# Kernel optimization log

Measured on AMD Instinct MI355X. Metric: run time of the kernel, lower is better.

## Reference

```python
import jax, jax.numpy as jnp
import numpy as np

# Model hyperparameters (match init_kwargs)
NUM_HEADS = 12
KEY_SIZE = 64
VALUE_SIZE = 64
D_MODEL = 768
NUM_LAYERS = 4
FFW = 3072
B, T, L = 2, 32, 256
LN_EPS = 1e-5


def _layer_norm(x, scale, offset):
    m = jnp.mean(x, axis=-1, keepdims=True)
    v = jnp.mean(jnp.square(x - m), axis=-1, keepdims=True)
    return (x - m) * jax.lax.rsqrt(v + LN_EPS) * scale + offset


def _axial_attn(x, Wq, Wk, Wv, Wo, bo, mode):
    # x: [B, T, L, D]
    b, t, l, d = x.shape
    q = (x @ Wq).reshape(b, t, l, NUM_HEADS, KEY_SIZE)
    k = (x @ Wk).reshape(b, t, l, NUM_HEADS, KEY_SIZE)
    v = (x @ Wv).reshape(b, t, l, NUM_HEADS, VALUE_SIZE)
    inv_sqrt_d = KEY_SIZE ** (-0.5)
    if mode == 'time':
        logits = jnp.einsum('btlhd,bTlhd->blhtT', q, k) * inv_sqrt_d
        w = jax.nn.softmax(logits, axis=-1)
        a = jnp.einsum('blhtT,bTlhd->btlhd', w, v)
    else:  # space
        logits = jnp.einsum('btlhd,btLhd->bthlL', q, k) * inv_sqrt_d
        w = jax.nn.softmax(logits, axis=-1)
        a = jnp.einsum('bthlL,btLhd->btlhd', w, v)
    a = a.reshape(b, t, l, NUM_HEADS * VALUE_SIZE)
    return a @ Wo + bo


def _forward(input_embeddings, Wq_t, Wk_t, Wv_t, Wo_t, bo_t,
             Wq_s, Wk_s, Wv_s, Wo_s, bo_s,
             ln_t_scale, ln_t_bias, ln_s_scale, ln_s_bias,
             ln2_scale, ln2_bias, W1, b1, W2, b2):
    def block(h, p):
        (wq_t, wk_t, wv_t, wo_t, bot, wq_s, wk_s, wv_s, wo_s, bos,
         lts, ltb, lss, lsb, l2s, l2b, w1, bb1, w2, bb2) = p
        # time attention + residual
        x = _layer_norm(h, lts, ltb)
        h = h + _axial_attn(x, wq_t, wk_t, wv_t, wo_t, bot, 'time')
        # space attention + residual
        x = _layer_norm(h, lss, lsb)
        h = h + _axial_attn(x, wq_s, wk_s, wv_s, wo_s, bos, 'space')
        # FFN + residual
        x = _layer_norm(h, l2s, l2b)
        ff = jax.nn.gelu(x @ w1 + bb1) @ w2 + bb2
        return h + ff, None

    params = (Wq_t, Wk_t, Wv_t, Wo_t, bo_t, Wq_s, Wk_s, Wv_s, Wo_s, bo_s,
              ln_t_scale, ln_t_bias, ln_s_scale, ln_s_bias,
              ln2_scale, ln2_bias, W1, b1, W2, b2)
    h, _ = jax.lax.scan(block, input_embeddings, params)
    return h


def setup_inputs() -> dict:
    key = jax.random.key(0)
    ks = jax.random.split(key, 32)
    D, H, KD, VD, F, NL = D_MODEL, NUM_HEADS, KEY_SIZE, VALUE_SIZE, FFW, NUM_LAYERS
    init_scale = 2.0 / np.sqrt(NL)  # VarianceScaling scale used by the module
    s_in = np.sqrt(init_scale / D).astype(np.float32)   # fan_in = D
    s_out = np.sqrt(init_scale / (H * VD)).astype(np.float32)
    s_ffw2 = np.sqrt(init_scale / F).astype(np.float32)
    x = jax.random.normal(ks[0], (B, T, L, D), dtype=jnp.float32)
    def nrm(k, shape, s):
        return jax.random.normal(k, shape, dtype=jnp.float32) * s
    inp = {
        'input_embeddings': x,
        'Wq_t': nrm(ks[1], (NL, D, H * KD), s_in),
        'Wk_t': nrm(ks[2], (NL, D, H * KD), s_in),
        'Wv_t': nrm(ks[3], (NL, D, H * VD), s_in),
        'Wo_t': nrm(ks[4], (NL, H * VD, D), s_out),
        'bo_t': jnp.zeros((NL, D), jnp.float32),
        'Wq_s': nrm(ks[5], (NL, D, H * KD), s_in),
        'Wk_s': nrm(ks[6], (NL, D, H * KD), s_in),
        'Wv_s': nrm(ks[7], (NL, D, H * VD), s_in),
        'Wo_s': nrm(ks[8], (NL, H * VD, D), s_out),
        'bo_s': jnp.zeros((NL, D), jnp.float32),
        'ln_t_scale': jnp.ones((NL, D), jnp.float32),
        'ln_t_bias': jnp.zeros((NL, D), jnp.float32),
        'ln_s_scale': jnp.ones((NL, D), jnp.float32),
        'ln_s_bias': jnp.zeros((NL, D), jnp.float32),
        'ln2_scale': jnp.ones((NL, D), jnp.float32),
        'ln2_bias': jnp.zeros((NL, D), jnp.float32),
        'W1': nrm(ks[9], (NL, D, F), s_in),
        'b1': jnp.zeros((NL, F), jnp.float32),
        'W2': nrm(ks[10], (NL, F, D), s_ffw2),
        'b2': jnp.zeros((NL, D), jnp.float32),
    }
    return inp


def reference(input_embeddings, Wq_t, Wk_t, Wv_t, Wo_t, bo_t,
              Wq_s, Wk_s, Wv_s, Wo_s, bo_s,
              ln_t_scale, ln_t_bias, ln_s_scale, ln_s_bias,
              ln2_scale, ln2_bias, W1, b1, W2, b2):
    return _forward(input_embeddings, Wq_t, Wk_t, Wv_t, Wo_t, bo_t,
                    Wq_s, Wk_s, Wv_s, Wo_s, bo_s,
                    ln_t_scale, ln_t_bias, ln_s_scale, ln_s_bias,
                    ln2_scale, ln2_bias, W1, b1, W2, b2)
```

## Files before the change

### kernel.cpp

```cpp
#include <hip/hip_runtime.h>


#define AS1 __attribute__((address_space(1)))
#define AS3 __attribute__((address_space(3)))

using bf16x8 = __attribute__((ext_vector_type(8))) short;
using f32x4  = __attribute__((ext_vector_type(4))) float;

__device__ __forceinline__ f32x4 mfma_bf16(bf16x8 a, bf16x8 b, f32x4 c) {
  return __builtin_amdgcn_mfma_f32_16x16x32_bf16(a, b, c, 0, 0, 0);
}

__device__ __forceinline__ void async16(const void* g, void* l) {
  __builtin_amdgcn_global_load_lds((const AS1 void*)g, (AS3 void*)l, 16, 0, 0);
}

__device__ __forceinline__ short f2bs(float f) {
  union { float f; unsigned u; } x; x.f = f;
  unsigned r = x.u + 0x7fffu + ((x.u >> 16) & 1u);
  return (short)(r >> 16);
}

__device__ __forceinline__ f32x4 fzero() {
  f32x4 v; v[0] = 0.f; v[1] = 0.f; v[2] = 0.f; v[3] = 0.f; return v;
}

__device__ __forceinline__ float quad16_max(float v) {
  v = fmaxf(v, __shfl_xor(v, 1));
  v = fmaxf(v, __shfl_xor(v, 2));
  v = fmaxf(v, __shfl_xor(v, 4));
  v = fmaxf(v, __shfl_xor(v, 8));
  return v;
}
__device__ __forceinline__ float quad16_sum(float v) {
  v += __shfl_xor(v, 1); v += __shfl_xor(v, 2);
  v += __shfl_xor(v, 4); v += __shfl_xor(v, 8);
  return v;
}

template<int MODE>
__global__ __launch_bounds__(256) void gemm_bt(
    const short* __restrict__ A, const short* __restrict__ BT,
    const float* __restrict__ bias, const float* __restrict__ resid,
    float* __restrict__ outF, short* __restrict__ outB,
    int M, int N, int K, int nx)
{
  __shared__ __align__(16) short lA[128 * 64];
  __shared__ __align__(16) short lB[128 * 64];
  const int tid  = threadIdx.x;
  const int wave = tid >> 6, lane = tid & 63;
  const int quad = lane >> 4, l16 = lane & 15;
  const int wm = wave >> 1, wn = wave & 1;

  const unsigned flat = blockIdx.x;
  const unsigned su = flat >> 3;
  const unsigned nxu = (unsigned)nx;
  const unsigned xt = su % nxu;
  const unsigned yt = (flat & 7u) + 8u * (su / nxu);
  const long bm0 = (long)yt * 128;
  const long bn0 = (long)xt * 128;

  const int srow = lane >> 3;
  const int skof = ((lane & 7) ^ srow) * 8;

  f32x4 acc[4][4];
#pragma unroll
  for (int i = 0; i < 4; ++i)
#pragma unroll
    for (int j = 0; j < 4; ++j) acc[i][j] = fzero();

  for (int k0 = 0; k0 < K; k0 += 64) {
    __syncthreads();
#pragma unroll
    for (int cc = 0; cc < 4; ++cc) {
      int c = wave * 4 + cc;
      long row = c * 8 + srow;
      async16(A  + (bm0 + row) * (long)K + k0 + skof, (char*)lA + c * 1024);
      async16(BT + (bn0 + row) * (long)K + k0 + skof, (char*)lB + c * 1024);
    }
    __syncthreads();
#pragma unroll
    for (int kk = 0; kk < 2; ++kk) {
      bf16x8 a[4], b[4];
      const int pg = ((kk * 4 + quad) ^ (l16 & 7)) * 8;
#pragma unroll
      for (int i = 0; i < 4; ++i)
        a[i] = *(const bf16x8*)&lA[(wm * 64 + i * 16 + l16) * 64 + pg];
#pragma unroll
      for (int j = 0; j < 4; ++j)
        b[j] = *(const bf16x8*)&lB[(wn * 64 + j * 16 + l16) * 64 + pg];
#pragma unroll
      for (int i = 0; i < 4; ++i)
#pragma unroll
        for (int j = 0; j < 4; ++j)
          acc[i][j] = mfma_bf16(a[i], b[j], acc[i][j]);
    }
  }

#pragma unroll
  for (int i = 0; i < 4; ++i)
#pragma unroll
    for (int j = 0; j < 4; ++j)
#pragma unroll
      for (int r = 0; r < 4; ++r) {
        long gr = bm0 + wm * 64 + i * 16 + quad * 4 + r;
        long gc = bn0 + wn * 64 + j * 16 + l16;
        size_t idx = (size_t)gr * N + gc;
        float v = acc[i][j][r];
        if (MODE == 0) {
          outB[idx] = f2bs(v);
        } else if (MODE == 1) {
          outF[idx] = v + bias[gc] + resid[idx];
        } else {
          float t = v + bias[gc];
          float g = 0.5f * t * (1.f + tanhf(0.7978845608f * (t + 0.044715f * t * t * t)));
          outB[idx] = f2bs(g);
        }
      }
}

__global__ __launch_bounds__(256) void ln_kernel(
    const float* __restrict__ h, const float* __restrict__ sc,
    const float* __restrict__ bi, short* __restrict__ out)
{
  const int row = blockIdx.x, tid = threadIdx.x;
  const float* hr = h + (long)row * 768;
  float x0 = hr[tid], x1 = hr[tid + 256], x2 = hr[tid + 512];
  __shared__ float red[4];
  float s = x0 + x1 + x2;
#pragma unroll
  for (int m = 32; m >= 1; m >>= 1) s += __shfl_xor(s, m);
  if ((tid & 63) == 0) red[tid >> 6] = s;
  __syncthreads();
  float mean = (red[0] + red[1] + red[2] + red[3]) * (1.f / 768.f);
  float d0 = x0 - mean, d1 = x1 - mean, d2 = x2 - mean;
  float q = d0 * d0 + d1 * d1 + d2 * d2;
#pragma unroll
  for (int m = 32; m >= 1; m >>= 1) q += __shfl_xor(q, m);
  __syncthreads();
  if ((tid & 63) == 0) red[tid >> 6] = q;
  __syncthreads();
  float var = (red[0] + red[1] + red[2] + red[3]) * (1.f / 768.f);
  float inv = rsqrtf(var + 1e-5f);
  long o = (long)row * 768;
  out[o + tid]       = f2bs(d0 * inv * sc[tid]       + bi[tid]);
  out[o + tid + 256] = f2bs(d1 * inv * sc[tid + 256] + bi[tid + 256]);
  out[o + tid + 512] = f2bs(d2 * inv * sc[tid + 512] + bi[tid + 512]);
}

__global__ __launch_bounds__(256) void transpose_w(
    const float* __restrict__ in, short* __restrict__ out, int Kd, int Nd)
{
  __shared__ float t[32][33];
  const int n0 = blockIdx.x * 32, k0 = blockIdx.y * 32;
  const int r = threadIdx.x >> 5, c = threadIdx.x & 31;
#pragma unroll
  for (int rr = 0; rr < 4; ++rr)
    t[r + rr * 8][c] = in[(long)(k0 + r + rr * 8) * Nd + n0 + c];
  __syncthreads();
#pragma unroll
  for (int rr = 0; rr < 4; ++rr)
    out[(long)(n0 + r + rr * 8) * Kd + k0 + c] = f2bs(t[c][r + rr * 8]);
}

__global__ __launch_bounds__(256) void attn_space(
    const short* __restrict__ qkv, short* __restrict__ ao)
{
  __shared__ __align__(16) short VT[64 * 256];
  __shared__ __align__(16) short P[4][16 * 256];
  const int qt = blockIdx.x, hh = blockIdx.y, bt = blockIdx.z;
  const long tok0 = (long)bt * 256;
  const int tid = threadIdx.x, wave = tid >> 6, lane = tid & 63;
  const int quad = lane >> 4, l16 = lane & 15;

#pragma unroll
  for (int it = 0; it < 8; ++it) {
    int chunk = it * 256 + tid;
    int vl = chunk >> 3, d8 = (chunk & 7) * 8;
    bf16x8 v = *(const bf16x8*)(qkv + (tok0 + vl) * 2304 + 1536 + hh * 64 + d8);
#pragma unroll
    for (int e = 0; e < 8; ++e) VT[(d8 + e) * 256 + vl] = v[e];
  }

  const int qr = qt * 64 + wave * 16;
  bf16x8 qf[2];
#pragma unroll
  for (int kk = 0; kk < 2; ++kk)
    qf[kk] = *(const bf16x8*)(qkv + (tok0 + qr + l16) * 2304 + hh * 64 + kk * 32 + quad * 8);

  f32x4 S[16];
#pragma unroll
  for (int j = 0; j < 16; ++j) S[j] = fzero();
#pragma unroll
  for (int j = 0; j < 16; ++j)
#pragma unroll
    for (int kk = 0; kk < 2; ++kk) {
      bf16x8 kf = *(const bf16x8*)(qkv + (tok0 + j * 16 + l16) * 2304 + 768 + hh * 64 + kk * 32 + quad * 8);
      S[j] = mfma_bf16(qf[kk], kf, S[j]);
    }

#pragma unroll
  for (int r = 0; r < 4; ++r) {
    float m = -1e30f;
#pragma unroll
    for (int j = 0; j < 16; ++j) m = fmaxf(m, S[j][r]);
    m = quad16_max(m);
    float sum = 0.f;
#pragma unroll
    for (int j = 0; j < 16; ++j) {
      float e = __expf((S[j][r] - m) * 0.125f);
      S[j][r] = e; sum += e;
    }
    sum = quad16_sum(sum);
    float inv = 1.f / sum;
#pragma unroll
    for (int j = 0; j < 16; ++j)
      P[wave][(quad * 4 + r) * 256 + j * 16 + l16] = f2bs(S[j][r] * inv);
  }
  __syncthreads();

  f32x4 O[4];
#pragma unroll
  for (int jn = 0; jn < 4; ++jn) O[jn] = fzero();
  for (int kk = 0; kk < 8; ++kk) {
    bf16x8 pf = *(const bf16x8*)&P[wave][l16 * 256 + kk * 32 + quad * 8];
#pragma unroll
    for (int jn = 0; jn < 4; ++jn) {
      bf16x8 vf = *(const bf16x8*)&VT[(jn * 16 + l16) * 256 + kk * 32 + quad * 8];
      O[jn] = mfma_bf16(pf, vf, O[jn]);
    }
  }
#pragma unroll
  for (int jn = 0; jn < 4; ++jn)
#pragma unroll
    for (int r = 0; r < 4; ++r) {
      int row = qr + quad * 4 + r;
      ao[(tok0 + row) * 768 + hh * 64 + jn * 16 + l16] = f2bs(O[jn][r]);
    }
}

__global__ __launch_bounds__(64) void attn_time(
    const short* __restrict__ qkv, short* __restrict__ ao)
{
  __shared__ __align__(16) short VT[64 * 32];
  __shared__ __align__(16) short P[32 * 32];
  const int ll = blockIdx.x, hh = blockIdx.y, b = blockIdx.z;
  const int lane = threadIdx.x;
  const int quad = lane >> 4, l16 = lane & 15;
#define TOK(t) (((long)(b * 32 + (t))) * 256 + ll)

#pragma unroll
  for (int it = 0; it < 4; ++it) {
    int chunk = it * 64 + lane;
    int t = chunk >> 3, d8 = (chunk & 7) * 8;
    bf16x8 v = *(const bf16x8*)(qkv + TOK(t) * 2304 + 1536 + hh * 64 + d8);
#pragma unroll
    for (int e = 0; e < 8; ++e) VT[(d8 + e) * 32 + t] = v[e];
  }

  bf16x8 qf[2][2];
#pragma unroll
  for (int mi = 0; mi < 2; ++mi)
#pragma unroll
    for (int kk = 0; kk < 2; ++kk)
      qf[mi][kk] = *(const bf16x8*)(qkv + TOK(mi * 16 + l16) * 2304 + hh * 64 + kk * 32 + quad * 8);

  f32x4 S[2][2];
#pragma unroll
  for (int mi = 0; mi < 2; ++mi) { S[mi][0] = fzero(); S[mi][1] = fzero(); }
#pragma unroll
  for (int nj = 0; nj < 2; ++nj)
#pragma unroll
    for (int kk = 0; kk < 2; ++kk) {
      bf16x8 kf = *(const bf16x8*)(qkv + TOK(nj * 16 + l16) * 2304 + 768 + hh * 64 + kk * 32 + quad * 8);
#pragma unroll
      for (int mi = 0; mi < 2; ++mi)
        S[mi][nj] = mfma_bf16(qf[mi][kk], kf, S[mi][nj]);
    }

#pragma unroll
  for (int mi = 0; mi < 2; ++mi)
#pragma unroll
    for (int r = 0; r < 4; ++r) {
      float m = fmaxf(S[mi][0][r], S[mi][1][r]);
      m = quad16_max(m);
      float e0 = __expf((S[mi][0][r] - m) * 0.125f);
      float e1 = __expf((S[mi][1][r] - m) * 0.125f);
      float sum = quad16_sum(e0 + e1);
      float inv = 1.f / sum;
      P[(mi * 16 + quad * 4 + r) * 32 + l16]      = f2bs(e0 * inv);
      P[(mi * 16 + quad * 4 + r) * 32 + 16 + l16] = f2bs(e1 * inv);
    }
  __syncthreads();

  f32x4 O[2][4];
#pragma unroll
  for (int mi = 0; mi < 2; ++mi)
#pragma unroll
    for (int jn = 0; jn < 4; ++jn) O[mi][jn] = fzero();
#pragma unroll
  for (int mi = 0; mi < 2; ++mi) {
    bf16x8 pf = *(const bf16x8*)&P[(mi * 16 + l16) * 32 + quad * 8];
#pragma unroll
    for (int jn = 0; jn < 4; ++jn) {
      bf16x8 vf = *(const bf16x8*)&VT[(jn * 16 + l16) * 32 + quad * 8];
      O[mi][jn] = mfma_bf16(pf, vf, O[mi][jn]);
    }
  }
#pragma unroll
  for (int mi = 0; mi < 2; ++mi)
#pragma unroll
    for (int jn = 0; jn < 4; ++jn)
#pragma unroll
      for (int r = 0; r < 4; ++r) {
        int t = mi * 16 + quad * 4 + r;
        ao[TOK(t) * 768 + hh * 64 + jn * 16 + l16] = f2bs(O[mi][jn][r]);
      }
#undef TOK
}

extern "C" void kernel_launch(void* const* d_in, const int* in_sizes, int n_in,
                              void* d_out, int out_size, void* d_ws, size_t ws_size,
                              hipStream_t stream)
{
  const float* emb     = (const float*)d_in[0];
  const float* Wq_t    = (const float*)d_in[1];
  const float* Wk_t    = (const float*)d_in[2];
  const float* Wv_t    = (const float*)d_in[3];
  const float* Wo_t    = (const float*)d_in[4];
  const float* bo_t    = (const float*)d_in[5];
  const float* Wq_s    = (const float*)d_in[6];
  const float* Wk_s    = (const float*)d_in[7];
  const float* Wv_s    = (const float*)d_in[8];
  const float* Wo_s    = (const float*)d_in[9];
  const float* bo_s    = (const float*)d_in[10];
  const float* ln_t_sc = (const float*)d_in[11];
  const float* ln_t_bi = (const float*)d_in[12];
  const float* ln_s_sc = (const float*)d_in[13];
  const float* ln_s_bi = (const float*)d_in[14];
  const float* ln2_sc  = (const float*)d_in[15];
  const float* ln2_bi  = (const float*)d_in[16];
  const float* W1      = (const float*)d_in[17];
  const float* b1      = (const float*)d_in[18];
  const float* W2      = (const float*)d_in[19];
  const float* b2      = (const float*)d_in[20];

  const long M = 16384, D = 768, QN = 2304, F = 3072;
  char* ws = (char*)d_ws;
  size_t off = 0;
  auto alloc = [&](size_t b) { char* p = ws + off; off += (b + 255) & ~(size_t)255; return p; };
  short* qkvT_t = (short*)alloc((size_t)4 * QN * D * 2);
  short* qkvT_s = (short*)alloc((size_t)4 * QN * D * 2);
  short* woT_t  = (short*)alloc((size_t)4 * D * D * 2);
  short* woT_s  = (short*)alloc((size_t)4 * D * D * 2);
  short* w1T    = (short*)alloc((size_t)4 * F * D * 2);
  short* w2T    = (short*)alloc((size_t)4 * D * F * 2);
  short* xb     = (short*)alloc((size_t)M * D * 2);
  short* aob    = (short*)alloc((size_t)M * D * 2);
  short* big    = (short*)alloc((size_t)M * F * 2);
  float* h = (float*)d_out;

  hipMemcpyAsync(h, emb, (size_t)M * D * 4, hipMemcpyDeviceToDevice, stream);

  for (int l = 0; l < 4; ++l) {
    const long wo = (long)l * D * D;
    transpose_w<<<dim3(24, 24), 256, 0, stream>>>(Wq_t + wo, qkvT_t + (long)l * QN * D,            768, 768);
    transpose_w<<<dim3(24, 24), 256, 0, stream>>>(Wk_t + wo, qkvT_t + (long)l * QN * D + D * D,    768, 768);
    transpose_w<<<dim3(24, 24), 256, 0, stream>>>(Wv_t + wo, qkvT_t + (long)l * QN * D + 2 * D * D, 768, 768);
    transpose_w<<<dim3(24, 24), 256, 0, stream>>>(Wq_s + wo, qkvT_s + (long)l * QN * D,            768, 768);
    transpose_w<<<dim3(24, 24), 256, 0, stream>>>(Wk_s + wo, qkvT_s + (long)l * QN * D + D * D,    768, 768);
    transpose_w<<<dim3(24, 24), 256, 0, stream>>>(Wv_s + wo, qkvT_s + (long)l * QN * D + 2 * D * D, 768, 768);
    transpose_w<<<dim3(24, 24), 256, 0, stream>>>(Wo_t + wo, woT_t + wo, 768, 768);
    transpose_w<<<dim3(24, 24), 256, 0, stream>>>(Wo_s + wo, woT_s + wo, 768, 768);
    transpose_w<<<dim3(96, 24), 256, 0, stream>>>(W1 + (long)l * D * F, w1T + (long)l * F * D, 768, 3072);
    transpose_w<<<dim3(24, 96), 256, 0, stream>>>(W2 + (long)l * F * D, w2T + (long)l * D * F, 3072, 768);
  }

  for (int l = 0; l < 4; ++l) {
    ln_kernel<<<16384, 256, 0, stream>>>(h, ln_t_sc + l * 768, ln_t_bi + l * 768, xb);
    gemm_bt<0><<<18 * 128, 256, 0, stream>>>(xb, qkvT_t + (long)l * QN * D,
        nullptr, nullptr, nullptr, big, 16384, 2304, 768, 18);
    attn_time<<<dim3(256, 12, 2), 64, 0, stream>>>(big, aob);
    gemm_bt<1><<<6 * 128, 256, 0, stream>>>(aob, woT_t + (long)l * D * D,
        bo_t + l * 768, h, h, nullptr, 16384, 768, 768, 6);
    ln_kernel<<<16384, 256, 0, stream>>>(h, ln_s_sc + l * 768, ln_s_bi + l * 768, xb);
    gemm_bt<0><<<18 * 128, 256, 0, stream>>>(xb, qkvT_s + (long)l * QN * D,
        nullptr, nullptr, nullptr, big, 16384, 2304, 768, 18);
    attn_space<<<dim3(4, 12, 64), 256, 0, stream>>>(big, aob);
    gemm_bt<1><<<6 * 128, 256, 0, stream>>>(aob, woT_s + (long)l * D * D,
        bo_s + l * 768, h, h, nullptr, 16384, 768, 768, 6);
    ln_kernel<<<16384, 256, 0, stream>>>(h, ln2_sc + l * 768, ln2_bi + l * 768, xb);
    gemm_bt<2><<<24 * 128, 256, 0, stream>>>(xb, w1T + (long)l * F * D,
        b1 + l * 3072, nullptr, nullptr, big, 16384, 3072, 768, 24);
    gemm_bt<1><<<6 * 128, 256, 0, stream>>>(big, w2T + (long)l * D * F,
        b2 + l * 768, h, h, nullptr, 16384, 768, 3072, 6);
  }
}
```

Baseline: 2.861 ms.

## Double-buffer GEMM LDS tiles with register prefetch and batch weight transposes

The GEMM main loop changes from direct global-to-LDS async loads over K=64 tiles, with two barriers per step, to K=32 tiles. These are loaded into registers one step ahead and stored into a padded, double-buffered LDS array, leaving a single barrier per step. The goal is to overlap global loads with MFMA work and cut synchronisation. The trade-off is twice as many K iterations and a loss of the hardware direct-to-LDS path. Separately, the 40 per-layer weight-transpose launches are merged into a few batched launches to reduce launch overhead.

```diff
diff --git a/kernel.cpp b/kernel.cpp
--- a/kernel.cpp
+++ b/kernel.cpp
@@ -1,18 +1,11 @@
 #include <hip/hip_runtime.h>
 
-
-#define AS1 __attribute__((address_space(1)))
-#define AS3 __attribute__((address_space(3)))
 
 using bf16x8 = __attribute__((ext_vector_type(8))) short;
 using f32x4  = __attribute__((ext_vector_type(4))) float;
 
 __device__ __forceinline__ f32x4 mfma_bf16(bf16x8 a, bf16x8 b, f32x4 c) {
   return __builtin_amdgcn_mfma_f32_16x16x32_bf16(a, b, c, 0, 0, 0);
-}
-
-__device__ __forceinline__ void async16(const void* g, void* l) {
-  __builtin_amdgcn_global_load_lds((const AS1 void*)g, (AS3 void*)l, 16, 0, 0);
 }
 
 __device__ __forceinline__ short f2bs(float f) {
@@ -38,6 +31,7 @@
   return v;
 }
 
+#define LSTR 40
 template<int MODE>
 __global__ __launch_bounds__(256) void gemm_bt(
     const short* __restrict__ A, const short* __restrict__ BT,
@@ -45,8 +39,8 @@
     float* __restrict__ outF, short* __restrict__ outB,
     int M, int N, int K, int nx)
 {
-  __shared__ __align__(16) short lA[128 * 64];
-  __shared__ __align__(16) short lB[128 * 64];
+  __shared__ __align__(16) short lA[2][128 * LSTR];
+  __shared__ __align__(16) short lB[2][128 * LSTR];
   const int tid  = threadIdx.x;
   const int wave = tid >> 6, lane = tid & 63;
   const int quad = lane >> 4, l16 = lane & 15;
@@ -60,8 +54,14 @@
   const long bm0 = (long)yt * 128;
   const long bn0 = (long)xt * 128;
 
-  const int srow = lane >> 3;
-  const int skof = ((lane & 7) ^ srow) * 8;
+  const int c0 = wave * 2;
+  const int srow = lane >> 2;
+  const int sg   = lane & 3;
+  const long arow0 = bm0 + c0 * 16 + srow;
+  const long brow0 = bn0 + c0 * 16 + srow;
+  const int  skk   = sg * 8;
+  const int wofs0 = (c0 * 16 + srow) * LSTR + sg * 8;
+  const int wofs1 = wofs0 + 16 * LSTR;
 
   f32x4 acc[4][4];
 #pragma unroll
@@ -69,31 +69,46 @@
 #pragma unroll
     for (int j = 0; j < 4; ++j) acc[i][j] = fzero();
 
-  for (int k0 = 0; k0 < K; k0 += 64) {
-    __syncthreads();
-#pragma unroll
-    for (int cc = 0; cc < 4; ++cc) {
-      int c = wave * 4 + cc;
-      long row = c * 8 + srow;
-      async16(A  + (bm0 + row) * (long)K + k0 + skof, (char*)lA + c * 1024);
-      async16(BT + (bn0 + row) * (long)K + k0 + skof, (char*)lB + c * 1024);
-    }
-    __syncthreads();
-#pragma unroll
-    for (int kk = 0; kk < 2; ++kk) {
-      bf16x8 a[4], b[4];
-      const int pg = ((kk * 4 + quad) ^ (l16 & 7)) * 8;
-#pragma unroll
-      for (int i = 0; i < 4; ++i)
-        a[i] = *(const bf16x8*)&lA[(wm * 64 + i * 16 + l16) * 64 + pg];
+  const int niter = K >> 5;
+
+  bf16x8 sa0 = *(const bf16x8*)(A  + arow0 * K + skk);
+  bf16x8 sa1 = *(const bf16x8*)(A  + (arow0 + 16) * K + skk);
+  bf16x8 sb0 = *(const bf16x8*)(BT + brow0 * K + skk);
+  bf16x8 sb1 = *(const bf16x8*)(BT + (brow0 + 16) * K + skk);
+  *(bf16x8*)&lA[0][wofs0] = sa0;
+  *(bf16x8*)&lA[0][wofs1] = sa1;
+  *(bf16x8*)&lB[0][wofs0] = sb0;
+  *(bf16x8*)&lB[0][wofs1] = sb1;
+  __syncthreads();
+
+  for (int k = 0; k < niter; ++k) {
+    const int cur = k & 1, nxt = cur ^ 1;
+    const bool more = (k + 1) < niter;
+    if (more) {
+      const long ko = (long)(k + 1) * 32 + skk;
+      sa0 = *(const bf16x8*)(A  + arow0 * K + ko);
+      sa1 = *(const bf16x8*)(A  + (arow0 + 16) * K + ko);
+      sb0 = *(const bf16x8*)(BT + brow0 * K + ko);
+      sb1 = *(const bf16x8*)(BT + (brow0 + 16) * K + ko);
+    }
+    bf16x8 a[4], b[4];
+#pragma unroll
+    for (int i = 0; i < 4; ++i)
+      a[i] = *(const bf16x8*)&lA[cur][(wm * 64 + i * 16 + l16) * LSTR + quad * 8];
+#pragma unroll
+    for (int j = 0; j < 4; ++j)
+      b[j] = *(const bf16x8*)&lB[cur][(wn * 64 + j * 16 + l16) * LSTR + quad * 8];
+#pragma unroll
+    for (int i = 0; i < 4; ++i)
 #pragma unroll
       for (int j = 0; j < 4; ++j)
-        b[j] = *(const bf16x8*)&lB[(wn * 64 + j * 16 + l16) * 64 + pg];
-#pragma unroll
-      for (int i = 0; i < 4; ++i)
-#pragma unroll
-        for (int j = 0; j < 4; ++j)
-          acc[i][j] = mfma_bf16(a[i], b[j], acc[i][j]);
+        acc[i][j] = mfma_bf16(a[i], b[j], acc[i][j]);
+    if (more) {
+      *(bf16x8*)&lA[nxt][wofs0] = sa0;
+      *(bf16x8*)&lA[nxt][wofs1] = sa1;
+      *(bf16x8*)&lB[nxt][wofs0] = sb0;
+      *(bf16x8*)&lB[nxt][wofs1] = sb1;
+      __syncthreads();
     }
   }
 
@@ -148,10 +163,31 @@
   out[o + tid + 512] = f2bs(d2 * inv * sc[tid + 512] + bi[tid + 512]);
 }
 
+struct TP8 { const float* src[8]; short* dst[8]; long sstride, dstride; };
+
+__global__ __launch_bounds__(256) void transpose768_all(TP8 p)
+{
+  __shared__ float t[32][33];
+  const int g = blockIdx.z >> 2, l = blockIdx.z & 3;
+  const float* in = p.src[g] + (long)l * 768 * 768;
+  short* out = p.dst[g] + (long)l * p.dstride;
+  const int n0 = blockIdx.x * 32, k0 = blockIdx.y * 32;
+  const int r = threadIdx.x >> 5, c = threadIdx.x & 31;
+#pragma unroll
+  for (int rr = 0; rr < 4; ++rr)
+    t[r + rr * 8][c] = in[(long)(k0 + r + rr * 8) * 768 + n0 + c];
+  __syncthreads();
+#pragma unroll
+  for (int rr = 0; rr < 4; ++rr)
+    out[(long)(n0 + r + rr * 8) * 768 + k0 + c] = f2bs(t[c][r + rr * 8]);
+}
+
 __global__ __launch_bounds__(256) void transpose_w(
-    const float* __restrict__ in, short* __restrict__ out, int Kd, int Nd)
+    const float* __restrict__ in0, short* __restrict__ out0, int Kd, int Nd)
 {
   __shared__ float t[32][33];
+  const float* in = in0 + (long)blockIdx.z * Kd * Nd;
+  short* out = out0 + (long)blockIdx.z * Kd * Nd;
   const int n0 = blockIdx.x * 32, k0 = blockIdx.y * 32;
   const int r = threadIdx.x >> 5, c = threadIdx.x & 31;
 #pragma unroll
@@ -362,19 +398,30 @@
 
   hipMemcpyAsync(h, emb, (size_t)M * D * 4, hipMemcpyDeviceToDevice, stream);
 
-  for (int l = 0; l < 4; ++l) {
-    const long wo = (long)l * D * D;
-    transpose_w<<<dim3(24, 24), 256, 0, stream>>>(Wq_t + wo, qkvT_t + (long)l * QN * D,            768, 768);
-    transpose_w<<<dim3(24, 24), 256, 0, stream>>>(Wk_t + wo, qkvT_t + (long)l * QN * D + D * D,    768, 768);
-    transpose_w<<<dim3(24, 24), 256, 0, stream>>>(Wv_t + wo, qkvT_t + (long)l * QN * D + 2 * D * D, 768, 768);
-    transpose_w<<<dim3(24, 24), 256, 0, stream>>>(Wq_s + wo, qkvT_s + (long)l * QN * D,            768, 768);
-    transpose_w<<<dim3(24, 24), 256, 0, stream>>>(Wk_s + wo, qkvT_s + (long)l * QN * D + D * D,    768, 768);
-    transpose_w<<<dim3(24, 24), 256, 0, stream>>>(Wv_s + wo, qkvT_s + (long)l * QN * D + 2 * D * D, 768, 768);
-    transpose_w<<<dim3(24, 24), 256, 0, stream>>>(Wo_t + wo, woT_t + wo, 768, 768);
-    transpose_w<<<dim3(24, 24), 256, 0, stream>>>(Wo_s + wo, woT_s + wo, 768, 768);
-    transpose_w<<<dim3(96, 24), 256, 0, stream>>>(W1 + (long)l * D * F, w1T + (long)l * F * D, 768, 3072);
-    transpose_w<<<dim3(24, 96), 256, 0, stream>>>(W2 + (long)l * F * D, w2T + (long)l * D * F, 3072, 768);
-  }
+  TP8 tp;
+  tp.src[0] = Wq_t; tp.dst[0] = qkvT_t;
+  tp.src[1] = Wk_t; tp.dst[1] = qkvT_t + D * D;
+  tp.src[2] = Wv_t; tp.dst[2] = qkvT_t + 2 * D * D;
+  tp.src[3] = Wq_s; tp.dst[3] = qkvT_s;
+  tp.src[4] = Wk_s; tp.dst[4] = qkvT_s + D * D;
+  tp.src[5] = Wv_s; tp.dst[5] = qkvT_s + 2 * D * D;
+  tp.src[6] = Wo_t; tp.dst[6] = woT_t;
+  tp.src[7] = Wo_s; tp.dst[7] = woT_s;
+  tp.sstride = D * D;
+  tp.dstride = 0;
+  TP8 tp_a = tp; tp_a.dstride = QN * D;
+  TP8 tp_b = tp; tp_b.dstride = D * D;
+  {
+    transpose768_all<<<dim3(24, 24, 24), 256, 0, stream>>>(tp_a);
+    TP8 tp_c;
+    tp_c.src[0] = Wo_t; tp_c.dst[0] = woT_t;
+    tp_c.src[1] = Wo_s; tp_c.dst[1] = woT_s;
+    for (int g = 2; g < 8; ++g) { tp_c.src[g] = Wo_t; tp_c.dst[g] = woT_t; }
+    tp_c.sstride = D * D; tp_c.dstride = D * D;
+    transpose768_all<<<dim3(24, 24, 8), 256, 0, stream>>>(tp_c);
+  }
+  transpose_w<<<dim3(96, 24, 4), 256, 0, stream>>>(W1, w1T, 768, 3072);
+  transpose_w<<<dim3(24, 96, 4), 256, 0, stream>>>(W2, w2T, 3072, 768);
 
   for (int l = 0; l < 4; ++l) {
     ln_kernel<<<16384, 256, 0, stream>>>(h, ln_t_sc + l * 768, ln_t_bi + l * 768, xb);
```

New measurement: 2.878 ms. No clear change (+0.6%).
